# Kernel optimization log

Hardware: AMD Instinct MI355X
Metric: run time of the kernel (lower is better)

The kernel has to match this reference:

```python
import jax, jax.numpy as jnp
import numpy as np

B, N, D = 512, 101, 128
H = D
NHEADS = 8
HD = H // NHEADS
NSTEPS = 140


def setup_inputs() -> dict:
    key = jax.random.key(0)
    ks = jax.random.split(key, 12)
    enc = jax.random.normal(ks[0], (B, N, D), jnp.float32)
    pool = jax.random.normal(ks[1], (B, H), jnp.float32)
    # CVRP-style demands: depot demand 0, customers in (0, 0.2); capacity normalized to 1.0
    demand = jax.random.uniform(ks[2], (B, N), jnp.float32) * 0.2
    demand = demand.at[:, 0].set(0.0)
    capcity = jnp.ones((B, 1), jnp.float32)
    actions_old = jax.random.randint(ks[3], (B, NSTEPS), 0, N, dtype=jnp.int32)

    def lin(k, fin, fout):
        return (jax.random.normal(k, (fin, fout), jnp.float32) / np.sqrt(fin)).astype(jnp.float32)

    return dict(
        encoder_inputs=enc, pool=pool, actions_old=actions_old,
        capcity=capcity, demand=demand, n_steps=NSTEPS, batch_size=B,
        W_fc=lin(ks[4], H + 1, H),      # Decoder1.fc  (no bias)
        W_fc1=lin(ks[5], H, H),         # Decoder1.fc1
        W_w=lin(ks[6], D, H),           # Attention1.w (cat=1)
        W_k=lin(ks[7], D, H),           # Attention1.k
        W_v=lin(ks[8], D, H),           # Attention1.v
        W_attnfc=lin(ks[9], H, H),      # Attention1.fc
        W_pk=lin(ks[10], D, H),         # ProbAttention.k
    )


def reference(encoder_inputs, pool, actions_old, capcity, demand, n_steps, batch_size,
              W_fc, W_fc1, W_w, W_k, W_v, W_attnfc, W_pk):
    Bs, Nn, Dd = encoder_inputs.shape
    Hh = W_fc.shape[1]
    nh = NHEADS
    hd = Hh // nh
    cap0 = capcity[0, 0]  # torch: capcity[0].item()
    demands = demand
    col = jnp.arange(Nn)

    # context is constant across decode steps -> hoist K/V/pointer-K projections
    Kh = (encoder_inputs @ W_k).reshape(Bs, Nn, nh, hd).transpose(0, 2, 1, 3)  # (B,h,N,hd)
    Vh = (encoder_inputs @ W_v).reshape(Bs, Nn, nh, hd).transpose(0, 2, 1, 3)
    Kp = encoder_inputs @ W_pk  # (B,N,H)

    def update_mask(mask1, dyn_cap, index):
        # mask1: visited nodes (bool). depot masked iff we just arrived at depot.
        go_depot = index == 0
        m1 = jnp.logical_or(mask1, col[None, :] == index[:, None])
        m1 = m1.at[:, 0].set(go_depot)
        mask = jnp.logical_or(m1, demands > dyn_cap)  # dyn_cap (B,1) broadcasts
        # guard: if everything masked (instance finished), allow depot (torch code
        # breaks out of the loop instead; log_p is zeroed by is_done either way)
        all_masked = jnp.all(mask, axis=1)
        mask = mask.at[:, 0].set(jnp.where(all_masked, False, mask[:, 0]))
        return mask, m1

    def update_state(dyn_cap, index):
        cur = jnp.take_along_axis(demands, index[:, None], axis=1)
        dyn = dyn_cap - cur
        return jnp.where((index == 0)[:, None], cap0, dyn)

    mask1_init = jnp.zeros((Bs, Nn), bool)
    idx0 = jnp.zeros((Bs,), jnp.int32)
    mask_init, mask1_init = update_mask(mask1_init, capcity, idx0)  # i == 0 update

    def step(carry, _):
        _input, dyn_cap, mask, mask1, pool_c = carry
        dec = jnp.concatenate([_input, dyn_cap], axis=-1) @ W_fc  # (B,H)
        pool_n = pool_c @ W_fc1                                   # pool re-projected EVERY step (as in torch)
        dec = dec + pool_n
        # --- Attention1 (multi-head glimpse) ---
        Q = (dec @ W_w).reshape(Bs, nh, hd)
        compat = jnp.einsum('bhd,bhnd->bhn', Q, Kh) * (1.0 / np.sqrt(hd))
        u = jnp.where(mask[:, None, :], -jnp.inf, compat)
        sc = jax.nn.softmax(u, axis=-1)
        glimpse = jnp.einsum('bhn,bhnd->bhd', sc, Vh).reshape(Bs, Hh) @ W_attnfc
        # --- ProbAttention (tanh-clipped pointer) ---
        comp2 = jnp.einsum('bh,bnh->bn', glimpse, Kp) * (1.0 / np.sqrt(Hh))
        logits = jnp.where(mask, -jnp.inf, 10.0 * jnp.tanh(comp2))
        logp_all = jax.nn.log_softmax(logits, axis=-1)
        index = jnp.argmax(logp_all, axis=-1)  # greedy decode
        log_p = jnp.take_along_axis(logp_all, index[:, None], axis=1)[:, 0]
        is_done = (jnp.sum(mask1[:, 1:].astype(jnp.int32), axis=1) >= (Nn - 1)).astype(log_p.dtype)
        log_p = log_p * (1.0 - is_done)
        dyn_new = jax.lax.stop_gradient(update_state(dyn_cap, index))  # torch .detach()
        mask_new, mask1_new = update_mask(mask1, dyn_new, index)
        inp_new = jnp.take_along_axis(encoder_inputs, index[:, None, None], axis=1)[:, 0, :]
        return (inp_new, dyn_new, mask_new, mask1_new, pool_n), (index, log_p)

    carry0 = (encoder_inputs[:, 0, :], capcity, mask_init, mask1_init, pool)
    _, (actions, log_ps) = jax.lax.scan(step, carry0, None, length=int(n_steps))
    actions = actions.T            # (B, n_steps)
    log_p = jnp.sum(log_ps, axis=0)  # (B,)
    return actions, log_p
```

## Files before the change

kernel.cpp:

```cpp
#include <hip/hip_runtime.h>
#include <math.h>

#define B_ 512
#define N_ 101
#define H_ 128
#define T_ 140
#define M37 0x1FFFFFFFFFull

#define BAR() asm volatile("s_waitcnt lgkmcnt(0)\n\ts_barrier" ::: "memory")
#define LGKM0() asm volatile("s_waitcnt lgkmcnt(0)" ::: "memory")

template <int CTRL, int RM>
__device__ __forceinline__ float dpp_max_step(float x) {
  int t = __builtin_amdgcn_update_dpp((int)0xFF800000, __float_as_int(x), CTRL, RM, 0xF, false);
  return fmaxf(x, __int_as_float(t));
}
template <int CTRL, int RM>
__device__ __forceinline__ float dpp_add_step(float x) {
  int t = __builtin_amdgcn_update_dpp(0, __float_as_int(x), CTRL, RM, 0xF, false);
  return x + __int_as_float(t);
}
__device__ __forceinline__ float wave_max64(float x) {
  x = dpp_max_step<0x111, 0xF>(x);
  x = dpp_max_step<0x112, 0xF>(x);
  x = dpp_max_step<0x114, 0xF>(x);
  x = dpp_max_step<0x118, 0xF>(x);
  x = dpp_max_step<0x142, 0xA>(x);
  x = dpp_max_step<0x143, 0xC>(x);
  return __int_as_float(__builtin_amdgcn_readlane(__float_as_int(x), 63));
}
__device__ __forceinline__ float wave_sum64(float x) {
  x = dpp_add_step<0x111, 0xF>(x);
  x = dpp_add_step<0x112, 0xF>(x);
  x = dpp_add_step<0x114, 0xF>(x);
  x = dpp_add_step<0x118, 0xF>(x);
  x = dpp_add_step<0x142, 0xA>(x);
  x = dpp_add_step<0x143, 0xC>(x);
  return __int_as_float(__builtin_amdgcn_readlane(__float_as_int(x), 63));
}

__device__ __forceinline__ void gemm_tile_dev(
    const float* A, const float* B, float* C, int cb, int transB, int tid)
{
  int cc = cb * 32 + (tid & 7) * 4;
  int r0 = tid >> 3;
  float4 acc0 = {0,0,0,0}, acc1 = {0,0,0,0}, acc2 = {0,0,0,0}, acc3 = {0,0,0,0};
  for (int k = 0; k < 128; ++k) {
    float4 b4;
    if (!transB) {
      b4 = *(const float4*)(B + k * 128 + cc);
    } else {
      b4.x = B[(cc + 0) * 128 + k];
      b4.y = B[(cc + 1) * 128 + k];
      b4.z = B[(cc + 2) * 128 + k];
      b4.w = B[(cc + 3) * 128 + k];
    }
    float a0 = A[(r0 +  0) * 128 + k];
    float a1 = A[(r0 + 32) * 128 + k];
    float a2 = A[(r0 + 64) * 128 + k];
    float a3 = A[(r0 + 96) * 128 + k];
    acc0.x += a0 * b4.x; acc0.y += a0 * b4.y; acc0.z += a0 * b4.z; acc0.w += a0 * b4.w;
    acc1.x += a1 * b4.x; acc1.y += a1 * b4.y; acc1.z += a1 * b4.z; acc1.w += a1 * b4.w;
    acc2.x += a2 * b4.x; acc2.y += a2 * b4.y; acc2.z += a2 * b4.z; acc2.w += a2 * b4.w;
    acc3.x += a3 * b4.x; acc3.y += a3 * b4.y; acc3.z += a3 * b4.z; acc3.w += a3 * b4.w;
  }
  *(float4*)(C + (r0 +  0) * 128 + cc) = acc0;
  *(float4*)(C + (r0 + 32) * 128 + cc) = acc1;
  *(float4*)(C + (r0 + 64) * 128 + cc) = acc2;
  *(float4*)(C + (r0 + 96) * 128 + cc) = acc3;
}

__global__ __launch_bounds__(256) void stage_a(
    const float* __restrict__ Wfc, const float* __restrict__ Ww,
    const float* __restrict__ Wpk, const float* __restrict__ Wat,
    const float* __restrict__ F,
    float* __restrict__ Wfw, float* __restrict__ Wc, float* __restrict__ wcap,
    float* __restrict__ Mbuf)
{
  int j = blockIdx.x, tid = threadIdx.x;
  if (j < 4)       gemm_tile_dev(Wfc, Ww, Wfw, j, 0, tid);
  else if (j < 8)  gemm_tile_dev(Wpk, Wat, Wc, j - 4, 1, tid);
  else if (j == 8) {
    if (tid < 128) {
      float s = 0.f;
      for (int k = 0; k < 128; ++k) s += Wfc[128 * 128 + k] * Ww[k * 128 + tid];
      wcap[tid] = s;
    }
  } else gemm_tile_dev(F, F, Mbuf + 2ll * 16384, j - 9, 0, tid);
}

__global__ __launch_bounds__(256) void stage_b(
    const float* __restrict__ F, const float* __restrict__ enc,
    const float* __restrict__ Wfw, float* __restrict__ Mbuf,
    float* __restrict__ encW)
{
  int bx = blockIdx.x, tid = threadIdx.x;
  if (bx < 8) {
    int s = (bx >> 2) + 1, cb = bx & 3;
    const float* As = (s == 1) ? F : Mbuf + (long long)s * 16384;
    gemm_tile_dev(As, Mbuf + 2ll * 16384, Mbuf + (long long)(2 + s) * 16384, cb, 0, tid);
  } else {
    int jj = bx - 8, rb = jj >> 2, cb = jj & 3;
    gemm_tile_dev(enc + (long long)rb * 16384, Wfw, encW + (long long)rb * 16384, cb, 0, tid);
  }
}

__global__ __launch_bounds__(256) void chainL(
    const float* __restrict__ F, float* __restrict__ Mbuf, int L)
{
  int bx = blockIdx.x, tid = threadIdx.x;
  int s = (bx >> 2) + 1, cb = bx & 3;
  const float* As = (s == 1) ? F : Mbuf + (long long)s * 16384;
  gemm_tile_dev(As, Mbuf + (long long)L * 16384, Mbuf + (long long)(L + s) * 16384, cb, 0, tid);
}

__global__ __launch_bounds__(256) void stage_n8(
    const float* __restrict__ F, const float* __restrict__ Ww,
    float* __restrict__ Mbuf, float* __restrict__ Abuf)
{
  int bx = blockIdx.x, tid = threadIdx.x;
  if (bx < 48) {
    int s = (bx >> 2) + 1, cb = bx & 3;
    const float* As = (s == 1) ? F : Mbuf + (long long)s * 16384;
    gemm_tile_dev(As, Mbuf + 128ll * 16384, Mbuf + (long long)(128 + s) * 16384, cb, 0, tid);
  } else {
    int jj = bx - 48, t = jj >> 2, cb = jj & 3;
    const float* Ms = (t == 0) ? F : Mbuf + (long long)(t + 1) * 16384;
    gemm_tile_dev(Ms, Ww, Abuf + (long long)t * 16384, cb, 0, tid);
  }
}

__global__ __launch_bounds__(256) void stage_n9(
    const float* __restrict__ Ww, const float* __restrict__ pool,
    float* __restrict__ Mbuf, float* __restrict__ Abuf, float* __restrict__ Qpl)
{
  int bx = blockIdx.x, tid = threadIdx.x;
  if (bx < 52) {
    int t = 127 + (bx >> 2), cb = bx & 3;
    gemm_tile_dev(Mbuf + (long long)(t + 1) * 16384, Ww, Abuf + (long long)t * 16384, cb, 0, tid);
  } else {
    int jj = bx - 52, t = jj >> 4, sub = jj & 15, rb = sub >> 2, cb = sub & 3;
    gemm_tile_dev(pool + (long long)rb * 16384, Abuf + (long long)t * 16384,
                  Qpl + (long long)t * 65536 + (long long)rb * 16384, cb, 0, tid);
  }
}

__global__ __launch_bounds__(256) void stage_n10(
    const float* __restrict__ pool, float* __restrict__ Abuf, float* __restrict__ Qpl)
{
  int bx = blockIdx.x, tid = threadIdx.x;
  int t = 127 + (bx >> 4), sub = bx & 15, rb = sub >> 2, cb = sub & 3;
  gemm_tile_dev(pool + (long long)rb * 16384, Abuf + (long long)t * 16384,
                Qpl + (long long)t * 65536 + (long long)rb * 16384, cb, 0, tid);
}

__device__ __forceinline__ void compat_sm(
    int wave, int lane, int amaxU, float capU,
    unsigned long long msklo, unsigned long long mskhi,
    const float* s_buf, const float* s_wc, const float* s_qp,
    float* s_qs, const float* kreg, float* s_sc)
{
  if (lane < 32) {
    int d = (lane < 16) ? (wave * 16 + lane) : ((wave + 4) * 16 + (lane - 16));
    float qv = s_buf[amaxU * H_ + d] + capU * s_wc[d] + s_qp[d];
    s_qs[wave * 32 + lane] = qv;
  }
  LGKM0();
  const float4* q0 = (const float4*)(s_qs + wave * 32);
  const float4* q1 = (const float4*)(s_qs + wave * 32 + 16);
  float c00 = 0.f, c01 = 0.f, c10 = 0.f, c11 = 0.f;
#pragma unroll
  for (int q = 0; q < 4; ++q) {
    float4 qq = q0[q];
    c00 += qq.x * kreg[q * 4 + 0] + qq.y * kreg[q * 4 + 1]
         + qq.z * kreg[q * 4 + 2] + qq.w * kreg[q * 4 + 3];
    c10 += qq.x * kreg[32 + q * 4 + 0] + qq.y * kreg[32 + q * 4 + 1]
         + qq.z * kreg[32 + q * 4 + 2] + qq.w * kreg[32 + q * 4 + 3];
    float4 qr = q1[q];
    c01 += qr.x * kreg[16 + q * 4 + 0] + qr.y * kreg[16 + q * 4 + 1]
         + qr.z * kreg[16 + q * 4 + 2] + qr.w * kreg[16 + q * 4 + 3];
    c11 += qr.x * kreg[48 + q * 4 + 0] + qr.y * kreg[48 + q * 4 + 1]
         + qr.z * kreg[48 + q * 4 + 2] + qr.w * kreg[48 + q * 4 + 3];
  }
  bool mb0 = (msklo >> lane) & 1ull;
  bool mb1v = (lane < 37) ? ((mskhi >> lane) & 1ull) : true;
  float a0 = mb0 ? -INFINITY : 0.25f * c00;
  float a1 = mb0 ? -INFINITY : 0.25f * c01;
  float b0 = mb1v ? -INFINITY : 0.25f * c10;
  float b1 = mb1v ? -INFINITY : 0.25f * c11;

  float m0  = wave_max64(fmaxf(a0, b0));
  float m1v = wave_max64(fmaxf(a1, b1));
  float ea0 = expf(a0 - m0),  eb0 = (lane < 37) ? expf(b0 - m0)  : 0.f;
  float ea1 = expf(a1 - m1v), eb1 = (lane < 37) ? expf(b1 - m1v) : 0.f;
  float s0 = ea0 + eb0, s1 = ea1 + eb1;
#pragma unroll
  for (int off = 32; off > 0; off >>= 1) {
    s0 += __shfl_xor(s0, off);
    s1 += __shfl_xor(s1, off);
  }
  float* r0 = s_sc + wave * 104;
  float* r1 = s_sc + (wave + 4) * 104;
  r0[lane] = ea0 / s0; r1[lane] = ea1 / s1;
  if (lane < 37) { r0[64 + lane] = eb0 / s0; r1[64 + lane] = eb1 / s1; }
}

__global__ __attribute__((amdgpu_flat_work_group_size(256, 256), amdgpu_waves_per_eu(2, 2)))
void decode_kernel(
    const float* __restrict__ enc,
    const float* __restrict__ Wk,
    const float* __restrict__ Wv,
    const float* __restrict__ Wc,
    const float* __restrict__ encW,
    const float* __restrict__ Qpool,
    const float* __restrict__ wcap,
    const float* __restrict__ capcity,
    const float* __restrict__ demand,
    float* __restrict__ out)
{
  __shared__ __align__(16) float s_buf[N_ * 132];
  __shared__ __align__(16) float s_sc[8 * 104];
  __shared__ __align__(16) float s_part[256];
  __shared__ __align__(16) float s_p2[256];
  __shared__ __align__(16) float s_qs[128];
  __shared__ __align__(16) float s_wc[128];
  __shared__ __align__(16) float s_qp[128];

  const int b    = blockIdx.x;
  const int tid  = threadIdx.x;
  const int lane = tid & 63;
  const int wave = tid >> 6;
  const int an = tid & 127, aj = tid >> 7;
  const int bh2 = (lane >> 4) & 1;
  const int bj2 = (wave + ((lane >= 32) ? 4 : 0)) * 16 + (lane & 15);
  const float invSqrtH = 0.08838834764831845f;

  float cap  = capcity[b];
  float cap0 = capcity[0];
  float dem0 = demand[(long long)b * N_ + lane];
  float dem1 = (lane < 37) ? demand[(long long)b * N_ + 64 + lane] : 0.f;
  float wcr  = (tid < 128) ? wcap[tid] : 0.f;
  float qp0  = (tid < 128) ? Qpool[(long long)b * H_ + tid] : 0.f;

  for (int idx = tid; idx < N_ * 32; idx += 256) {
    int row = idx >> 5, q = idx & 31;
    float4 v = *(const float4*)(enc + ((long long)b * N_ + row) * H_ + q * 4);
    float* d = s_buf + row * 132 + q * 4;
    d[0] = v.x; d[1] = v.y; d[2] = v.z; d[3] = v.w;
  }
  BAR();

  float vreg[51];
#pragma unroll
  for (int q = 0; q < 51; ++q) vreg[q] = 0.f;
  {
    const int base = bh2 * 51;
    for (int i4 = 0; i4 < 32; ++i4) {
      float w0 = Wv[(i4 * 4 + 0) * H_ + bj2];
      float w1 = Wv[(i4 * 4 + 1) * H_ + bj2];
      float w2 = Wv[(i4 * 4 + 2) * H_ + bj2];
      float w3 = Wv[(i4 * 4 + 3) * H_ + bj2];
#pragma unroll
      for (int nl = 0; nl < 51; ++nl) {
        if (base + nl < N_) {
          float4 e = *(const float4*)(s_buf + (base + nl) * 132 + i4 * 4);
          vreg[nl] += e.x * w0 + e.y * w1 + e.z * w2 + e.w * w3;
        }
      }
    }
  }

  float kreg[64];
#pragma unroll
  for (int q = 0; q < 64; ++q) kreg[q] = 0.f;
  {
    const int n0 = lane;
    const int n1c = (lane < 37) ? 64 + lane : 0;
    for (int i = 0; i < 128; ++i) {
      float e0 = s_buf[n0 * 132 + i];
      float e1 = s_buf[n1c * 132 + i];
      const float4* wk0 = (const float4*)(Wk + i * H_ + wave * 16);
      const float4* wk1 = (const float4*)(Wk + i * H_ + (wave + 4) * 16);
#pragma unroll
      for (int q = 0; q < 4; ++q) {
        float4 a = wk0[q];
        kreg[q * 4 + 0] += e0 * a.x; kreg[q * 4 + 1] += e0 * a.y;
        kreg[q * 4 + 2] += e0 * a.z; kreg[q * 4 + 3] += e0 * a.w;
        kreg[32 + q * 4 + 0] += e1 * a.x; kreg[32 + q * 4 + 1] += e1 * a.y;
        kreg[32 + q * 4 + 2] += e1 * a.z; kreg[32 + q * 4 + 3] += e1 * a.w;
        float4 c = wk1[q];
        kreg[16 + q * 4 + 0] += e0 * c.x; kreg[16 + q * 4 + 1] += e0 * c.y;
        kreg[16 + q * 4 + 2] += e0 * c.z; kreg[16 + q * 4 + 3] += e0 * c.w;
        kreg[48 + q * 4 + 0] += e1 * c.x; kreg[48 + q * 4 + 1] += e1 * c.y;
        kreg[48 + q * 4 + 2] += e1 * c.z; kreg[48 + q * 4 + 3] += e1 * c.w;
      }
    }
  }

  float preg[64];
#pragma unroll
  for (int q = 0; q < 64; ++q) preg[q] = 0.f;
  if (an < N_) {
    for (int i = 0; i < 128; ++i) {
      float e = s_buf[an * 132 + i];
      const float4* wc = (const float4*)(Wc + i * H_ + aj * 64);
#pragma unroll
      for (int q = 0; q < 16; ++q) {
        float4 c = wc[q];
        preg[q * 4 + 0] += e * c.x; preg[q * 4 + 1] += e * c.y;
        preg[q * 4 + 2] += e * c.z; preg[q * 4 + 3] += e * c.w;
      }
    }
  }
  BAR();

  for (int idx = tid; idx < N_ * 32; idx += 256) {
    int row = idx >> 5, q = idx & 31;
    float4 v = *(const float4*)(encW + ((long long)b * N_ + row) * H_ + q * 4);
    float* d = s_buf + row * 128 + q * 4;
    d[0] = v.x; d[1] = v.y; d[2] = v.z; d[3] = v.w;
  }
  if (tid < 128) { s_wc[tid] = wcr; s_qp[tid] = qp0; }
  BAR();

  unsigned long long m1lo = 1ull, m1hi = 0ull;
  unsigned long long msklo, mskhi;
  {
    bool p0i = (lane == 0) || (dem0 > cap);
    bool p1i = (lane < 37) ? (dem1 > cap) : true;
    msklo = __ballot(p0i);
    mskhi = __ballot(p1i) & M37;
    if (msklo == ~0ull && mskhi == M37) msklo &= ~1ull;
  }
  float logpAcc = 0.f;
  compat_sm(wave, lane, 0, cap, msklo, mskhi, s_buf, s_wc, s_qp, s_qs, kreg, s_sc);

  for (int t = 0; t < T_; ++t) {
    int tn = (t + 1 < T_) ? (t + 1) : t;
    float qn = (tid < 128) ? Qpool[((long long)tn * B_ + b) * H_ + tid] : 0.f;

    {
      LGKM0();
      const float* srow = s_sc + (bj2 >> 4) * 104;
      float acc = 0.f;
      if (bh2 == 0) {
#pragma unroll
        for (int q = 0; q < 12; ++q) {
          float4 sv = *(const float4*)(srow + q * 4);
          acc += sv.x * vreg[q * 4 + 0] + sv.y * vreg[q * 4 + 1]
               + sv.z * vreg[q * 4 + 2] + sv.w * vreg[q * 4 + 3];
        }
        acc += srow[48] * vreg[48] + srow[49] * vreg[49] + srow[50] * vreg[50];
      } else {
        acc += srow[51] * vreg[0];
#pragma unroll
        for (int q = 0; q < 12; ++q) {
          float4 sv = *(const float4*)(srow + 52 + q * 4);
          acc += sv.x * vreg[1 + q * 4] + sv.y * vreg[2 + q * 4]
               + sv.z * vreg[3 + q * 4] + sv.w * vreg[4 + q * 4];
        }
        acc += srow[100] * vreg[49];
      }
      s_part[bh2 * 128 + bj2] = acc;
    }
    BAR();

    if (an < N_) {
      const float4* p0 = (const float4*)(s_part + aj * 64);
      const float4* p1 = (const float4*)(s_part + 128 + aj * 64);
      float c = 0.f;
#pragma unroll
      for (int q = 0; q < 16; ++q) {
        float4 g0 = p0[q], g1 = p1[q];
        float gx = g0.x + g1.x, gy = g0.y + g1.y, gz = g0.z + g1.z, gw = g0.w + g1.w;
        c += gx * preg[q * 4 + 0] + gy * preg[q * 4 + 1]
           + gz * preg[q * 4 + 2] + gw * preg[q * 4 + 3];
      }
      s_p2[aj * 128 + an] = c;
    }
    if (tid < 128) s_qp[tid] = qn;
    BAR();

    {
      float l0 = -INFINITY, l1 = -INFINITY;
      bool mb0 = (msklo >> lane) & 1ull;
      if (!mb0) l0 = 10.f * tanhf((s_p2[lane] + s_p2[128 + lane]) * invSqrtH);
      if (lane < 37) {
        bool mb1 = (mskhi >> lane) & 1ull;
        if (!mb1) l1 = 10.f * tanhf((s_p2[64 + lane] + s_p2[192 + lane]) * invSqrtH);
      }
      float vmax = wave_max64(fmaxf(l0, l1));
      unsigned long long blo = __ballot(l0 == vmax);
      unsigned long long bhi = __ballot(l1 == vmax);
      int amax = blo ? (__ffsll((long long)blo) - 1)
                     : (64 + __ffsll((long long)bhi) - 1);
      float ss = wave_sum64(__expf(l0 - vmax) + __expf(l1 - vmax));
      logpAcc -= __logf(ss);

      float dlo = __int_as_float(__builtin_amdgcn_readlane(__float_as_int(dem0), amax & 63));
      float dhi = __int_as_float(__builtin_amdgcn_readlane(__float_as_int(dem1), amax & 63));
      float capNew = (amax == 0) ? cap0 : (cap - ((amax < 64) ? dlo : dhi));
      if (amax < 64) m1lo |= (1ull << amax); else m1hi |= (1ull << (amax - 64));
      m1lo = (m1lo & ~1ull) | (unsigned long long)(amax == 0);
      bool doneNew = ((int)__popcll(m1lo & ~1ull) + (int)__popcll(m1hi)) >= (N_ - 1);
      bool p0m = ((m1lo >> lane) & 1ull) || (dem0 > capNew);
      bool p1m = (lane < 37) ? (((m1hi >> lane) & 1ull) || (dem1 > capNew)) : true;
      unsigned long long klo = __ballot(p0m);
      unsigned long long khi = __ballot(p1m) & M37;
      if (klo == ~0ull && khi == M37) klo &= ~1ull;
      msklo = klo; mskhi = khi; cap = capNew;

      if (tid == 0) out[(long long)b * T_ + t] = (float)amax;
      if (doneNew) {
        for (int tt = t + 1 + tid; tt < T_; tt += 256)
          out[(long long)b * T_ + tt] = 0.f;
        break;
      }
      if (t + 1 < T_)
        compat_sm(wave, lane, amax, capNew, msklo, mskhi,
                  s_buf, s_wc, s_qp, s_qs, kreg, s_sc);
    }
  }

  if (tid == 0) out[(long long)B_ * T_ + b] = logpAcc;
}

extern "C" void kernel_launch(void* const* d_in, const int* in_sizes, int n_in,
                              void* d_out, int out_size, void* d_ws, size_t ws_size,
                              hipStream_t stream)
{
  const float* enc   = (const float*)d_in[0];
  const float* pool  = (const float*)d_in[1];
  const float* cap   = (const float*)d_in[3];
  const float* dem   = (const float*)d_in[4];
  const float* W_fc  = (const float*)d_in[7];
  const float* W_fc1 = (const float*)d_in[8];
  const float* W_w   = (const float*)d_in[9];
  const float* W_kk  = (const float*)d_in[10];
  const float* W_vv  = (const float*)d_in[11];
  const float* W_at  = (const float*)d_in[12];
  const float* W_pk  = (const float*)d_in[13];
  float* out = (float*)d_out;
  float* ws  = (float*)d_ws;

  float* Mbuf  = ws;
  float* Abuf  = Mbuf + 141 * 16384;
  float* Qpl   = Abuf + 140 * 16384;
  float* encW  = Qpl + 140 * 512 * 128;
  float* Wfw   = encW + 512 * 101 * 128;
  float* Wc    = Wfw + 16384;
  float* wcapb = Wc + 16384;

  stage_a<<<13, 256, 0, stream>>>(W_fc, W_w, W_pk, W_at, W_fc1, Wfw, Wc, wcapb, Mbuf);
  stage_b<<<1624, 256, 0, stream>>>(W_fc1, enc, Wfw, Mbuf, encW);
  chainL<<<16, 256, 0, stream>>>(W_fc1, Mbuf, 4);
  chainL<<<32, 256, 0, stream>>>(W_fc1, Mbuf, 8);
  chainL<<<64, 256, 0, stream>>>(W_fc1, Mbuf, 16);
  chainL<<<128, 256, 0, stream>>>(W_fc1, Mbuf, 32);
  chainL<<<256, 256, 0, stream>>>(W_fc1, Mbuf, 64);
  stage_n8<<<556, 256, 0, stream>>>(W_fc1, W_w, Mbuf, Abuf);
  stage_n9<<<2084, 256, 0, stream>>>(W_w, pool, Mbuf, Abuf, Qpl);
  stage_n10<<<208, 256, 0, stream>>>(pool, Abuf, Qpl);
  decode_kernel<<<512, 256, 0, stream>>>(enc, W_kk, W_vv, Wc, encW, Qpl, wcapb, cap, dem, out);
}
```

Measured before the change: 1.043 ms.

## Vectorize GEMM tile loads, fuse query build into compat, use DPP butterfly reductions

The setup GEMM tile now reads A and B as float4 over four k values per iteration, including the transposed-B path. The compat routine builds the query on the fly from vectorized LDS reads, which drops the s_qs scratch buffer and one LDS wait. The xor-shuffle sum is replaced by a ds_swizzle plus DPP butterfly. The log-sum-exp accumulation now runs only in wave 0, which is the wave that writes the output. Together these aim to cut LDS traffic and cross-lane latency on the serial decode path, at the cost of a redundant query computation in every lane.

```diff
diff --git a/kernel.cpp b/kernel.cpp
--- a/kernel.cpp
+++ b/kernel.cpp
@@ -39,30 +39,69 @@
   return __int_as_float(__builtin_amdgcn_readlane(__float_as_int(x), 63));
 }
 
+__device__ __forceinline__ float bfly_xor16(float x) {
+  return __int_as_float(__builtin_amdgcn_ds_swizzle(__float_as_int(x), 0x401F));
+}
+__device__ __forceinline__ float bfly_xor8(float x) {
+  int xi = __float_as_int(x);
+  int t = __builtin_amdgcn_update_dpp(xi, xi, 0x128, 0xF, 0xF, false);
+  return __int_as_float(t);
+}
+__device__ __forceinline__ float bfly_xor4(float x) {
+  int xi = __float_as_int(x);
+  int t = __builtin_amdgcn_update_dpp(xi, xi, 0x104, 0xF, 0x5, false);
+  t = __builtin_amdgcn_update_dpp(t, xi, 0x114, 0xF, 0xA, false);
+  return __int_as_float(t);
+}
+__device__ __forceinline__ float bfly_xor2(float x) {
+  int xi = __float_as_int(x);
+  int t = __builtin_amdgcn_update_dpp(xi, xi, 0x4E, 0xF, 0xF, false);
+  return __int_as_float(t);
+}
+__device__ __forceinline__ float bfly_xor1(float x) {
+  int xi = __float_as_int(x);
+  int t = __builtin_amdgcn_update_dpp(xi, xi, 0xB1, 0xF, 0xF, false);
+  return __int_as_float(t);
+}
+
 __device__ __forceinline__ void gemm_tile_dev(
     const float* A, const float* B, float* C, int cb, int transB, int tid)
 {
   int cc = cb * 32 + (tid & 7) * 4;
   int r0 = tid >> 3;
   float4 acc0 = {0,0,0,0}, acc1 = {0,0,0,0}, acc2 = {0,0,0,0}, acc3 = {0,0,0,0};
-  for (int k = 0; k < 128; ++k) {
-    float4 b4;
+  for (int k4 = 0; k4 < 32; ++k4) {
+    const int k = k4 * 4;
+    float4 a0v = *(const float4*)(A + (r0 +  0) * 128 + k);
+    float4 a1v = *(const float4*)(A + (r0 + 32) * 128 + k);
+    float4 a2v = *(const float4*)(A + (r0 + 64) * 128 + k);
+    float4 a3v = *(const float4*)(A + (r0 + 96) * 128 + k);
+    float4 b0, b1, b2, b3;
     if (!transB) {
-      b4 = *(const float4*)(B + k * 128 + cc);
+      b0 = *(const float4*)(B + (k + 0) * 128 + cc);
+      b1 = *(const float4*)(B + (k + 1) * 128 + cc);
+      b2 = *(const float4*)(B + (k + 2) * 128 + cc);
+      b3 = *(const float4*)(B + (k + 3) * 128 + cc);
     } else {
-      b4.x = B[(cc + 0) * 128 + k];
-      b4.y = B[(cc + 1) * 128 + k];
-      b4.z = B[(cc + 2) * 128 + k];
-      b4.w = B[(cc + 3) * 128 + k];
-    }
-    float a0 = A[(r0 +  0) * 128 + k];
-    float a1 = A[(r0 + 32) * 128 + k];
-    float a2 = A[(r0 + 64) * 128 + k];
-    float a3 = A[(r0 + 96) * 128 + k];
-    acc0.x += a0 * b4.x; acc0.y += a0 * b4.y; acc0.z += a0 * b4.z; acc0.w += a0 * b4.w;
-    acc1.x += a1 * b4.x; acc1.y += a1 * b4.y; acc1.z += a1 * b4.z; acc1.w += a1 * b4.w;
-    acc2.x += a2 * b4.x; acc2.y += a2 * b4.y; acc2.z += a2 * b4.z; acc2.w += a2 * b4.w;
-    acc3.x += a3 * b4.x; acc3.y += a3 * b4.y; acc3.z += a3 * b4.z; acc3.w += a3 * b4.w;
+      float4 t0 = *(const float4*)(B + (cc + 0) * 128 + k);
+      float4 t1 = *(const float4*)(B + (cc + 1) * 128 + k);
+      float4 t2 = *(const float4*)(B + (cc + 2) * 128 + k);
+      float4 t3 = *(const float4*)(B + (cc + 3) * 128 + k);
+      b0 = make_float4(t0.x, t1.x, t2.x, t3.x);
+      b1 = make_float4(t0.y, t1.y, t2.y, t3.y);
+      b2 = make_float4(t0.z, t1.z, t2.z, t3.z);
+      b3 = make_float4(t0.w, t1.w, t2.w, t3.w);
+    }
+#define GSTEP(AC, BV) \
+    acc0.x += a0v.AC * BV.x; acc0.y += a0v.AC * BV.y; acc0.z += a0v.AC * BV.z; acc0.w += a0v.AC * BV.w; \
+    acc1.x += a1v.AC * BV.x; acc1.y += a1v.AC * BV.y; acc1.z += a1v.AC * BV.z; acc1.w += a1v.AC * BV.w; \
+    acc2.x += a2v.AC * BV.x; acc2.y += a2v.AC * BV.y; acc2.z += a2v.AC * BV.z; acc2.w += a2v.AC * BV.w; \
+    acc3.x += a3v.AC * BV.x; acc3.y += a3v.AC * BV.y; acc3.z += a3v.AC * BV.z; acc3.w += a3v.AC * BV.w;
+    GSTEP(x, b0)
+    GSTEP(y, b1)
+    GSTEP(z, b2)
+    GSTEP(w, b3)
+#undef GSTEP
   }
   *(float4*)(C + (r0 +  0) * 128 + cc) = acc0;
   *(float4*)(C + (r0 + 32) * 128 + cc) = acc1;
@@ -158,25 +197,34 @@
     int wave, int lane, int amaxU, float capU,
     unsigned long long msklo, unsigned long long mskhi,
     const float* s_buf, const float* s_wc, const float* s_qp,
-    float* s_qs, const float* kreg, float* s_sc)
-{
-  if (lane < 32) {
-    int d = (lane < 16) ? (wave * 16 + lane) : ((wave + 4) * 16 + (lane - 16));
-    float qv = s_buf[amaxU * H_ + d] + capU * s_wc[d] + s_qp[d];
-    s_qs[wave * 32 + lane] = qv;
-  }
-  LGKM0();
-  const float4* q0 = (const float4*)(s_qs + wave * 32);
-  const float4* q1 = (const float4*)(s_qs + wave * 32 + 16);
+    const float* kreg, float* s_sc)
+{
+  const float* eb = s_buf + amaxU * H_;
+  const int d0 = wave * 16;
+  const int d1 = (wave + 4) * 16;
   float c00 = 0.f, c01 = 0.f, c10 = 0.f, c11 = 0.f;
 #pragma unroll
   for (int q = 0; q < 4; ++q) {
-    float4 qq = q0[q];
+    float4 e0 = *(const float4*)(eb + d0 + q * 4);
+    float4 w0 = *(const float4*)(s_wc + d0 + q * 4);
+    float4 p0 = *(const float4*)(s_qp + d0 + q * 4);
+    float4 qq;
+    qq.x = e0.x + capU * w0.x + p0.x;
+    qq.y = e0.y + capU * w0.y + p0.y;
+    qq.z = e0.z + capU * w0.z + p0.z;
+    qq.w = e0.w + capU * w0.w + p0.w;
     c00 += qq.x * kreg[q * 4 + 0] + qq.y * kreg[q * 4 + 1]
          + qq.z * kreg[q * 4 + 2] + qq.w * kreg[q * 4 + 3];
     c10 += qq.x * kreg[32 + q * 4 + 0] + qq.y * kreg[32 + q * 4 + 1]
          + qq.z * kreg[32 + q * 4 + 2] + qq.w * kreg[32 + q * 4 + 3];
-    float4 qr = q1[q];
+    float4 e1 = *(const float4*)(eb + d1 + q * 4);
+    float4 w1 = *(const float4*)(s_wc + d1 + q * 4);
+    float4 p1 = *(const float4*)(s_qp + d1 + q * 4);
+    float4 qr;
+    qr.x = e1.x + capU * w1.x + p1.x;
+    qr.y = e1.y + capU * w1.y + p1.y;
+    qr.z = e1.z + capU * w1.z + p1.z;
+    qr.w = e1.w + capU * w1.w + p1.w;
     c01 += qr.x * kreg[16 + q * 4 + 0] + qr.y * kreg[16 + q * 4 + 1]
          + qr.z * kreg[16 + q * 4 + 2] + qr.w * kreg[16 + q * 4 + 3];
     c11 += qr.x * kreg[48 + q * 4 + 0] + qr.y * kreg[48 + q * 4 + 1]
@@ -194,11 +242,12 @@
   float ea0 = expf(a0 - m0),  eb0 = (lane < 37) ? expf(b0 - m0)  : 0.f;
   float ea1 = expf(a1 - m1v), eb1 = (lane < 37) ? expf(b1 - m1v) : 0.f;
   float s0 = ea0 + eb0, s1 = ea1 + eb1;
-#pragma unroll
-  for (int off = 32; off > 0; off >>= 1) {
-    s0 += __shfl_xor(s0, off);
-    s1 += __shfl_xor(s1, off);
-  }
+  { float t0 = __shfl_xor(s0, 32), t1 = __shfl_xor(s1, 32); s0 += t0; s1 += t1; }
+  { float t0 = bfly_xor16(s0),     t1 = bfly_xor16(s1);     s0 += t0; s1 += t1; }
+  { float t0 = bfly_xor8(s0),      t1 = bfly_xor8(s1);      s0 += t0; s1 += t1; }
+  { float t0 = bfly_xor4(s0),      t1 = bfly_xor4(s1);      s0 += t0; s1 += t1; }
+  { float t0 = bfly_xor2(s0),      t1 = bfly_xor2(s1);      s0 += t0; s1 += t1; }
+  { float t0 = bfly_xor1(s0),      t1 = bfly_xor1(s1);      s0 += t0; s1 += t1; }
   float* r0 = s_sc + wave * 104;
   float* r1 = s_sc + (wave + 4) * 104;
   r0[lane] = ea0 / s0; r1[lane] = ea1 / s1;
@@ -222,7 +271,6 @@
   __shared__ __align__(16) float s_sc[8 * 104];
   __shared__ __align__(16) float s_part[256];
   __shared__ __align__(16) float s_p2[256];
-  __shared__ __align__(16) float s_qs[128];
   __shared__ __align__(16) float s_wc[128];
   __shared__ __align__(16) float s_qp[128];
 
@@ -333,7 +381,7 @@
     if (msklo == ~0ull && mskhi == M37) msklo &= ~1ull;
   }
   float logpAcc = 0.f;
-  compat_sm(wave, lane, 0, cap, msklo, mskhi, s_buf, s_wc, s_qp, s_qs, kreg, s_sc);
+  compat_sm(wave, lane, 0, cap, msklo, mskhi, s_buf, s_wc, s_qp, kreg, s_sc);
 
   for (int t = 0; t < T_; ++t) {
     int tn = (t + 1 < T_) ? (t + 1) : t;
@@ -394,8 +442,10 @@
       unsigned long long bhi = __ballot(l1 == vmax);
       int amax = blo ? (__ffsll((long long)blo) - 1)
                      : (64 + __ffsll((long long)bhi) - 1);
-      float ss = wave_sum64(__expf(l0 - vmax) + __expf(l1 - vmax));
-      logpAcc -= __logf(ss);
+      if (wave == 0) {
+        float ss = wave_sum64(__expf(l0 - vmax) + __expf(l1 - vmax));
+        logpAcc -= __logf(ss);
+      }
 
       float dlo = __int_as_float(__builtin_amdgcn_readlane(__float_as_int(dem0), amax & 63));
       float dhi = __int_as_float(__builtin_amdgcn_readlane(__float_as_int(dem1), amax & 63));
@@ -418,7 +468,7 @@
       }
       if (t + 1 < T_)
         compat_sm(wave, lane, amax, capNew, msklo, mskhi,
-                  s_buf, s_wc, s_qp, s_qs, kreg, s_sc);
+                  s_buf, s_wc, s_qp, kreg, s_sc);
     }
   }
 
```

Result: slower. 1.264 ms (+21.2%).
